# Kernel optimization log

Hardware: AMD Instinct MI355X
Metric: run time of the kernel (lower is better)

The kernel has to match this reference:

```python
import jax, jax.numpy as jnp
import numpy as np

L, H, NH, KVH, HD, DFF = 8, 1024, 16, 2, 64, 4096
G = NH // KVH          # kv groups = 8
S, PAST = 256, 2048
T = S + PAST
QKH = NH + KVH         # heads that receive RoPE


def setup_inputs() -> dict:
    key = jax.random.key(0)
    ks = jax.random.split(key, 10)
    w = 0.02
    # causal additive mask: past fully visible, causal within new chunk
    pos = jnp.arange(T)[None, :]
    mask = jnp.where(pos <= PAST + jnp.arange(S)[:, None], 0.0, -1e9).astype(jnp.float32)
    return {
        "hidden_states": jax.random.normal(ks[0], (S, H), jnp.float32),
        "rope_cos": jax.random.uniform(ks[1], (S, 1, HD), jnp.float32, -1.0, 1.0),
        "rope_sin": jax.random.uniform(ks[2], (S, 1, HD), jnp.float32, -1.0, 1.0),
        "attention_mask": mask,
        "past_keys": jax.random.normal(ks[3], (L, KVH, HD, PAST), jnp.float32),
        "past_values": jax.random.normal(ks[4], (L, KVH, PAST, HD), jnp.float32),
        "qkv_w": jax.random.normal(ks[5], (L, (NH + 2 * KVH) * HD, H), jnp.float32) * w,
        "o_w": jax.random.normal(ks[6], (L, H, H), jnp.float32) * w,
        "gate_up_w": jax.random.normal(ks[7], (L, 2 * DFF, H), jnp.float32) * w,
        "down_w": jax.random.normal(ks[8], (L, H, DFF), jnp.float32) * w,
        "norm_w": jnp.ones((H,), jnp.float32),
    }


def _rms_sum(x):
    # faithful to module: rsqrt of SUM of squares (sqrt(H) absorbed into fused weights)
    return x * jax.lax.rsqrt(jnp.sum(x * x, axis=-1, keepdims=True))


def _rotate_half(x):
    # flip-based rotate: swaps halves, NO negation (sign folded into sin input)
    return jnp.concatenate([x[..., HD // 2:], x[..., : HD // 2]], axis=-1)


def reference(hidden_states, rope_cos, rope_sin, attention_mask,
              past_keys, past_values, qkv_w, o_w, gate_up_w, down_w, norm_w):
    def layer(h, p):
        qw, ow, guw, dw, pk, pv = p
        # --- attention ---
        x = _rms_sum(h)
        qkv = (x @ qw.T).reshape(S, NH + 2 * KVH, HD)
        qk, v = qkv[:, :QKH], qkv[:, QKH:]               # [S,QKH,HD], [S,KVH,HD]
        qk = qk * rope_cos + _rotate_half(qk) * rope_sin
        q, k = qk[:, :NH], qk[:, NH:]
        q = q.reshape(S, KVH, G, HD).transpose(1, 2, 0, 3)       # [KVH,G,S,HD]
        K = jnp.concatenate([pk, k.transpose(1, 2, 0)], axis=-1)  # [KVH,HD,T]
        V = jnp.concatenate([pv, v.transpose(1, 0, 2)], axis=-2)  # [KVH,T,HD]
        scores = jnp.einsum('kgsd,kdt->kgst', q, K) + attention_mask
        p_attn = jax.nn.softmax(scores, axis=-1)
        o = jnp.einsum('kgst,ktd->kgsd', p_attn, V)
        o = o.transpose(2, 0, 1, 3).reshape(S, H)
        h = h + o @ ow.T
        # --- fused gate-up MLP (SiLU) ---
        x = _rms_sum(h)
        gu = x @ guw.T
        gate, up = gu[:, :DFF], gu[:, DFF:]
        h = h + (jax.nn.silu(gate) * up) @ dw.T
        return h, (K, V)

    h, _kv = jax.lax.scan(layer, hidden_states,
                          (qkv_w, o_w, gate_up_w, down_w, past_keys, past_values))
    # final RMSNorm (standard, mean-based, with learned weight)
    out = h * jax.lax.rsqrt(jnp.mean(h * h, axis=-1, keepdims=True) + 1e-6) * norm_w
    return out
```

## Files before the change

kernel.cpp:

```cpp
#include <hip/hip_runtime.h>
#include <hip/hip_bf16.h>

typedef __attribute__((ext_vector_type(4))) float f32x4;
typedef __attribute__((ext_vector_type(8))) __bf16 bf16x8;
typedef unsigned short u16;
typedef __attribute__((ext_vector_type(4))) unsigned short u16x4;
typedef __attribute__((ext_vector_type(8))) unsigned short u16x8;

__device__ __forceinline__ u16 f2bf(float f) {
  __bf16 h = (__bf16)f;
  return __builtin_bit_cast(u16, h);
}

__device__ __forceinline__ bf16x8 cvt2(f32x4 x, f32x4 y) {
  bf16x8 r;
  r[0] = (__bf16)x[0]; r[1] = (__bf16)x[1]; r[2] = (__bf16)x[2]; r[3] = (__bf16)x[3];
  r[4] = (__bf16)y[0]; r[5] = (__bf16)y[1]; r[6] = (__bf16)y[2]; r[7] = (__bf16)y[3];
  return r;
}

template<int CMODE, int NBK>
__global__ __launch_bounds__(512) void gemmW(
    const u16* __restrict__ A, const float* __restrict__ B,
    void* __restrict__ Cv, int K, int ldc)
{
  __shared__ char Bl[2][8192];
  int n0 = blockIdx.x * 32;
  int kb = blockIdx.y * (NBK * 128);
  int tid = threadIdx.x, lane = tid & 63, w = tid >> 6;
  int r0 = lane & 15, g = lane >> 4;
  int trow = tid >> 4, tcol = tid & 15;

  const float* bsrc = B + (long long)(n0 + trow) * K + kb + tcol * 8;
  const u16* abase = A + (long long)(w * 32 + r0) * K + kb + g * 8;
  int swr = (trow & 7) << 4;
  int wofs = trow * 256 + ((tcol * 16) ^ swr);

  {
    f32x4 u = *(const f32x4*)bsrc;
    f32x4 v = *(const f32x4*)(bsrc + 4);
    *(bf16x8*)&Bl[0][wofs] = cvt2(u, v);
  }
  bf16x8 a[2][2][4];
#pragma unroll
  for (int mi = 0; mi < 2; mi++)
#pragma unroll
    for (int kk = 0; kk < 4; kk++)
      a[0][mi][kk] = *(const bf16x8*)(abase + (long long)mi * 16 * K + kk * 32);

  f32x4 acc[2][2];
#pragma unroll
  for (int i = 0; i < 2; i++)
#pragma unroll
    for (int j = 0; j < 2; j++) acc[i][j] = (f32x4){0.f, 0.f, 0.f, 0.f};

  __syncthreads();

#pragma unroll
  for (int ibk = 0; ibk < NBK; ibk++) {
    const int cur = ibk & 1;
    const int nxt = cur ^ 1;
    f32x4 u, v;
    if (ibk + 1 < NBK) {
      int ko = (ibk + 1) * 128;
#pragma unroll
      for (int mi = 0; mi < 2; mi++)
#pragma unroll
        for (int kk = 0; kk < 4; kk++)
          a[nxt][mi][kk] = *(const bf16x8*)(abase + (long long)mi * 16 * K + ko + kk * 32);
      u = *(const f32x4*)(bsrc + ko);
      v = *(const f32x4*)(bsrc + ko + 4);
    }
    bf16x8 bfr[2][4];
#pragma unroll
    for (int nj = 0; nj < 2; nj++) {
      int row = nj * 16 + r0;
      int rb = row * 256, sw = (row & 7) << 4;
#pragma unroll
      for (int kk = 0; kk < 4; kk++)
        bfr[nj][kk] = *(const bf16x8*)&Bl[cur][rb + ((kk * 64 + g * 16) ^ sw)];
    }
#pragma unroll
    for (int kk = 0; kk < 4; kk++)
#pragma unroll
      for (int mi = 0; mi < 2; mi++)
#pragma unroll
        for (int nj = 0; nj < 2; nj++)
          acc[mi][nj] = __builtin_amdgcn_mfma_f32_16x16x32_bf16(a[cur][mi][kk], bfr[nj][kk], acc[mi][nj], 0, 0, 0);
    if (ibk + 1 < NBK)
      *(bf16x8*)&Bl[nxt][wofs] = cvt2(u, v);
    __syncthreads();
  }

  long long co = (long long)blockIdx.y * 256 * ldc;
  int rr = (lane >> 4) << 2;
#pragma unroll
  for (int mi = 0; mi < 2; mi++)
#pragma unroll
    for (int nj = 0; nj < 2; nj++)
#pragma unroll
      for (int q = 0; q < 4; q++) {
        int row = w * 32 + mi * 16 + rr + q;
        long long idx = co + (long long)row * ldc + n0 + nj * 16 + r0;
        float vv = acc[mi][nj][q];
        if (CMODE == 0) ((float*)Cv)[idx] = vv;
        else            ((u16*)Cv)[idx] = f2bf(vv);
      }
}

__global__ __launch_bounds__(256) void rms_fuse(const float* __restrict__ src,
                                                const float* __restrict__ parts, int np,
                                                float* __restrict__ hout, u16* __restrict__ x) {
  int s = blockIdx.x, tid = threadIdx.x;
  __shared__ float red[4];
  f32x4 hv = ((const f32x4*)(src + s * 1024))[tid];
  for (int p = 0; p < np; p++) {
    f32x4 pv = ((const f32x4*)(parts + (long long)p * 262144 + s * 1024))[tid];
    hv[0] += pv[0]; hv[1] += pv[1]; hv[2] += pv[2]; hv[3] += pv[3];
  }
  float ss = hv[0]*hv[0] + hv[1]*hv[1] + hv[2]*hv[2] + hv[3]*hv[3];
#pragma unroll
  for (int off = 32; off > 0; off >>= 1) ss += __shfl_xor(ss, off, 64);
  int lane = tid & 63, w = tid >> 6;
  if (lane == 0) red[w] = ss;
  __syncthreads();
  ss = red[0] + red[1] + red[2] + red[3];
  float r = 1.0f / sqrtf(ss);
  ((f32x4*)(hout + s * 1024))[tid] = hv;
  u16x4 o;
#pragma unroll
  for (int c = 0; c < 4; c++) o[c] = f2bf(hv[c] * r);
  ((u16x4*)x)[s * 256 + tid] = o;
}

__global__ __launch_bounds__(256) void final_fuse(const float* __restrict__ src,
                                                  const float* __restrict__ parts, int np,
                                                  const float* __restrict__ nw,
                                                  float* __restrict__ out) {
  int s = blockIdx.x, tid = threadIdx.x;
  __shared__ float red[4];
  f32x4 hv = ((const f32x4*)(src + s * 1024))[tid];
  for (int p = 0; p < np; p++) {
    f32x4 pv = ((const f32x4*)(parts + (long long)p * 262144 + s * 1024))[tid];
    hv[0] += pv[0]; hv[1] += pv[1]; hv[2] += pv[2]; hv[3] += pv[3];
  }
  float ss = hv[0]*hv[0] + hv[1]*hv[1] + hv[2]*hv[2] + hv[3]*hv[3];
#pragma unroll
  for (int off = 32; off > 0; off >>= 1) ss += __shfl_xor(ss, off, 64);
  int lane = tid & 63, w = tid >> 6;
  if (lane == 0) red[w] = ss;
  __syncthreads();
  ss = red[0] + red[1] + red[2] + red[3];
  float r = 1.0f / sqrtf(ss * (1.0f / 1024.0f) + 1e-6f);
  f32x4 wv = ((const f32x4*)nw)[tid];
  f32x4 o; o[0]=hv[0]*r*wv[0]; o[1]=hv[1]*r*wv[1]; o[2]=hv[2]*r*wv[2]; o[3]=hv[3]*r*wv[3];
  ((f32x4*)(out + s * 1024))[tid] = o;
}

__global__ __launch_bounds__(256) void transpose_past(const float* __restrict__ pk,
                                                      const float* __restrict__ pv,
                                                      u16* __restrict__ Kb, u16* __restrict__ Vb) {
  __shared__ float tile[64][65];
  int t0 = blockIdx.x * 64;
  int kvh = blockIdx.y;
  int l = blockIdx.z >> 1, part = blockIdx.z & 1;
  int lk = l * 2 + kvh;
  int tid = threadIdx.x;
  if (part == 0) {
    const float* src = pk + (long long)lk * 64 * 2048;
#pragma unroll
    for (int r = 0; r < 16; r++) {
      int idx = r * 256 + tid; int d = idx >> 6, t = idx & 63;
      tile[d][t] = src[d * 2048 + t0 + t];
    }
    __syncthreads();
    u16* dst = Kb + (long long)lk * 2304 * 64;
#pragma unroll
    for (int r = 0; r < 16; r++) {
      int idx = r * 256 + tid; int t = idx >> 6, d = idx & 63;
      dst[(t0 + t) * 64 + d] = f2bf(tile[d][t]);
    }
  } else {
    const float* src = pv + (long long)lk * 2048 * 64;
#pragma unroll
    for (int r = 0; r < 16; r++) {
      int idx = r * 256 + tid; int t = idx >> 6, d = idx & 63;
      tile[t][d] = src[(t0 + t) * 64 + d];
    }
    __syncthreads();
    u16* dst = Vb + (long long)lk * 64 * 2304;
#pragma unroll
    for (int r = 0; r < 16; r++) {
      int idx = r * 256 + tid; int d = idx >> 6, t = idx & 63;
      dst[d * 2304 + t0 + t] = f2bf(tile[t][d]);
    }
  }
}

__global__ __launch_bounds__(256) void rope_qkv(const float* __restrict__ P,
                                                const float* __restrict__ cs,
                                                const float* __restrict__ sn,
                                                u16* __restrict__ qb,
                                                u16* __restrict__ Kb,
                                                u16* __restrict__ Vb) {
  int s = blockIdx.x, tid = threadIdx.x;
  const float* p0 = P + (long long)s * 1280;
  const float* p1 = P + 327680 + (long long)s * 1280;
  for (int i = tid; i < 1280; i += 256) {
    int hh = i >> 6, d = i & 63;
    float v = p0[i] + p1[i];
    if (hh < 18) {
      int j = (hh << 6) | ((d + 32) & 63);
      float vr = p0[j] + p1[j];
      v = v * cs[s * 64 + d] + vr * sn[s * 64 + d];
      if (hh < 16) qb[hh * (256 * 64) + s * 64 + d] = f2bf(v);
      else         Kb[(hh - 16) * (2304 * 64) + (2048 + s) * 64 + d] = f2bf(v);
    } else {
      Vb[(hh - 18) * (64 * 2304) + d * 2304 + 2048 + s] = f2bf(v);
    }
  }
}

struct KV { bf16x8 kf[2][2]; bf16x8 vf[4]; };

__global__ __launch_bounds__(256) void flash_attn(
    const u16* __restrict__ qb, const u16* __restrict__ Kb2,
    const u16* __restrict__ Vb2, u16* __restrict__ oacc)
{
  __shared__ u16 Plds[4][16][36];
  __shared__ float Osh[4][16][68];
  __shared__ float msh[4][16];
  __shared__ float lsh[4][16];

  int hh = blockIdx.y, kvh = hh >> 3;
  int s0 = blockIdx.x * 16;
  int tid = threadIdx.x, lane = tid & 63, w = tid >> 6;
  int g = lane >> 4, r0 = lane & 15;

  const u16* Q  = qb  + hh * (256 * 64);
  const u16* Kh = Kb2 + kvh * (2304 * 64);
  const u16* Vh = Vb2 + kvh * (64 * 2304);

  bf16x8 qf[2];
#pragma unroll
  for (int kk = 0; kk < 2; kk++)
    qf[kk] = *(const bf16x8*)(Q + (s0 + r0) * 64 + kk * 32 + g * 8);

  f32x4 O[4];
#pragma unroll
  for (int dj = 0; dj < 4; dj++) O[dj] = (f32x4){0.f, 0.f, 0.f, 0.f};
  float m = -1e30f, l = 0.f;

  int t0s = w * 576;

  auto loadkv = [&](KV& d, int t0) {
#pragma unroll
    for (int tj = 0; tj < 2; tj++)
#pragma unroll
      for (int kk = 0; kk < 2; kk++)
        d.kf[tj][kk] = *(const bf16x8*)(Kh + (t0 + tj * 16 + r0) * 64 + kk * 32 + g * 8);
#pragma unroll
    for (int dj = 0; dj < 4; dj++)
      d.vf[dj] = *(const bf16x8*)(Vh + (dj * 16 + r0) * 2304 + t0 + g * 8);
  };

  auto step = [&](KV& kv, int t0) {
    f32x4 sc[2];
#pragma unroll
    for (int tj = 0; tj < 2; tj++) {
      f32x4 z = (f32x4){0.f, 0.f, 0.f, 0.f};
      z = __builtin_amdgcn_mfma_f32_16x16x32_bf16(kv.kf[tj][0], qf[0], z, 0, 0, 0);
      z = __builtin_amdgcn_mfma_f32_16x16x32_bf16(kv.kf[tj][1], qf[1], z, 0, 0, 0);
      sc[tj] = z;
    }
    if (t0 + 31 > 2048 + s0) {
#pragma unroll
      for (int tj = 0; tj < 2; tj++)
#pragma unroll
        for (int q = 0; q < 4; q++) {
          int tg = t0 + tj * 16 + g * 4 + q;
          int sg = s0 + r0;
          if (tg > 2048 + sg) sc[tj][q] = -1e30f;
        }
    }
    float rm = -1e30f;
#pragma unroll
    for (int tj = 0; tj < 2; tj++)
#pragma unroll
      for (int q = 0; q < 4; q++) rm = fmaxf(rm, sc[tj][q]);
    rm = fmaxf(rm, __shfl_xor(rm, 16, 64));
    rm = fmaxf(rm, __shfl_xor(rm, 32, 64));
    float mn = fmaxf(m, rm);
    float sca = __expf(m - mn);
    float rs = 0.f;
#pragma unroll
    for (int tj = 0; tj < 2; tj++)
#pragma unroll
      for (int q = 0; q < 4; q++) {
        sc[tj][q] = __expf(sc[tj][q] - mn);
        rs += sc[tj][q];
      }
    rs += __shfl_xor(rs, 16, 64);
    rs += __shfl_xor(rs, 32, 64);
    l = l * sca + rs;
    m = mn;
#pragma unroll
    for (int dj = 0; dj < 4; dj++) {
      O[dj][0] *= sca; O[dj][1] *= sca; O[dj][2] *= sca; O[dj][3] *= sca;
    }
#pragma unroll
    for (int tj = 0; tj < 2; tj++) {
      u16x4 pw;
#pragma unroll
      for (int q = 0; q < 4; q++) pw[q] = f2bf(sc[tj][q]);
      *(u16x4*)&Plds[w][r0][tj * 16 + g * 4] = pw;
    }
    u16x4 plo = *(const u16x4*)&Plds[w][r0][g * 8];
    u16x4 phi = *(const u16x4*)&Plds[w][r0][g * 8 + 4];
    union { bf16x8 v; u16x4 h[2]; } pu;
    pu.h[0] = plo; pu.h[1] = phi;
#pragma unroll
    for (int dj = 0; dj < 4; dj++)
      O[dj] = __builtin_amdgcn_mfma_f32_16x16x32_bf16(kv.vf[dj], pu.v, O[dj], 0, 0, 0);
  };

  KV bufA, bufB;
  loadkv(bufA, t0s);
#pragma unroll 1
  for (int it = 0; it < 18; it += 2) {
    int t0 = t0s + it * 32;
    loadkv(bufB, t0 + 32);
    step(bufA, t0);
    if (it + 2 < 18) loadkv(bufA, t0 + 64);
    step(bufB, t0 + 32);
  }

#pragma unroll
  for (int dj = 0; dj < 4; dj++)
    *(f32x4*)&Osh[w][r0][dj * 16 + g * 4] = O[dj];
  if (g == 0) { msh[w][r0] = m; lsh[w][r0] = l; }
  __syncthreads();

  int row = tid >> 4, c0 = (tid & 15) * 4;
  float M = fmaxf(fmaxf(msh[0][row], msh[1][row]), fmaxf(msh[2][row], msh[3][row]));
  float L = 0.f;
  float a0 = 0.f, a1 = 0.f, a2 = 0.f, a3 = 0.f;
#pragma unroll
  for (int w4 = 0; w4 < 4; w4++) {
    float e = __expf(msh[w4][row] - M);
    L += lsh[w4][row] * e;
    f32x4 ov = *(const f32x4*)&Osh[w4][row][c0];
    a0 += e * ov[0]; a1 += e * ov[1]; a2 += e * ov[2]; a3 += e * ov[3];
  }
  float inv = 1.0f / L;
  u16x4 o4;
  o4[0] = f2bf(a0 * inv); o4[1] = f2bf(a1 * inv);
  o4[2] = f2bf(a2 * inv); o4[3] = f2bf(a3 * inv);
  *(u16x4*)(oacc + (long long)(s0 + row) * 1024 + hh * 64 + c0) = o4;
}

__global__ __launch_bounds__(256) void silu_mul(const u16* __restrict__ gu, u16* __restrict__ y) {
  int t = blockIdx.x * 256 + threadIdx.x;
  int s = t >> 9, i8 = (t & 511) * 8;
  bf16x8 gv = *(const bf16x8*)(gu + s * 8192 + i8);
  bf16x8 uv = *(const bf16x8*)(gu + s * 8192 + 4096 + i8);
  u16x8 o8;
#pragma unroll
  for (int c = 0; c < 8; c++) {
    float gg = (float)gv[c];
    float uu = (float)uv[c];
    o8[c] = f2bf((gg / (1.0f + __expf(-gg))) * uu);
  }
  *(u16x8*)(y + s * 4096 + i8) = o8;
}

extern "C" void kernel_launch(void* const* d_in, const int* in_sizes, int n_in,
                              void* d_out, int out_size, void* d_ws, size_t ws_size,
                              hipStream_t stream) {
  (void)in_sizes; (void)n_in; (void)out_size; (void)ws_size;
  const float* hs   = (const float*)d_in[0];
  const float* rc   = (const float*)d_in[1];
  const float* rs   = (const float*)d_in[2];
  const float* pk   = (const float*)d_in[4];
  const float* pv   = (const float*)d_in[5];
  const float* qkvw = (const float*)d_in[6];
  const float* ow   = (const float*)d_in[7];
  const float* guw  = (const float*)d_in[8];
  const float* dw   = (const float*)d_in[9];
  const float* nw   = (const float*)d_in[10];
  float* out = (float*)d_out;

  char* base = (char*)d_ws;
  float* h   = (float*)(base + 0);
  u16*  x    = (u16*)(base + 1048576);
  float* Pq  = (float*)(base + 1572864);
  float* Po  = (float*)(base + 4194304);
  float* Pd  = (float*)(base + 8388608);
  u16*  gu   = (u16*)(base + 16777216);
  u16*  y    = (u16*)(base + 20971520);
  u16*  oacc = (u16*)(base + 23068672);
  u16*  qb   = (u16*)(base + 23592960);
  u16*  Kb   = (u16*)(base + 24117248);
  u16*  Vb   = (u16*)(base + 28835840);

  transpose_past<<<dim3(32, 2, 16), 256, 0, stream>>>(pk, pv, Kb, Vb);

  for (int l = 0; l < 8; ++l) {
    u16* Kbl = Kb + (long long)l * 2 * 2304 * 64;
    u16* Vbl = Vb + (long long)l * 2 * 64 * 2304;

    if (l == 0)
      rms_fuse<<<256, 256, 0, stream>>>(hs, nullptr, 0, h, x);
    else
      rms_fuse<<<256, 256, 0, stream>>>(h, Pd, 8, h, x);

    gemmW<0, 4><<<dim3(40, 2), 512, 0, stream>>>(
        x, qkvw + (long long)l * 1310720, Pq, 1024, 1280);
    rope_qkv<<<256, 256, 0, stream>>>(Pq, rc, rs, qb, Kbl, Vbl);
    flash_attn<<<dim3(16, 16), 256, 0, stream>>>(qb, Kbl, Vbl, oacc);
    gemmW<0, 2><<<dim3(32, 4), 512, 0, stream>>>(
        oacc, ow + (long long)l * 1048576, Po, 1024, 1024);
    rms_fuse<<<256, 256, 0, stream>>>(h, Po, 4, h, x);
    gemmW<1, 8><<<dim3(256, 1), 512, 0, stream>>>(
        x, guw + (long long)l * 8388608, gu, 1024, 8192);
    silu_mul<<<512, 256, 0, stream>>>(gu, y);
    gemmW<0, 4><<<dim3(32, 8), 512, 0, stream>>>(
        y, dw + (long long)l * 4194304, Pd, 4096, 1024);
  }
  final_fuse<<<256, 256, 0, stream>>>(h, Pd, 8, nw, out);
}
```

Before: 700.8 us.

## Fuse whole decoder stack into one cooperative persistent megakernel with grid barriers

Replaces the roughly 80 separate kernel launches (transpose, rms, gemms, rope, attention, silu) with one cooperative 256-block kernel. Phases are separated by atomic grid-wide barriers. The split-K and tiling layouts are reshaped to give 256 work units per phase, the SiLU multiply is fused into the gate-up GEMM epilogue, and attention uses 8 waves per block. This removes per-launch overhead and the intermediate gate-up buffer, at the cost of barrier spin latency and some idle blocks in phases with fewer tiles (QKV GEMM uses 160).

```diff
diff --git a/kernel.cpp b/kernel.cpp
--- a/kernel.cpp
+++ b/kernel.cpp
@@ -5,7 +5,6 @@
 typedef __attribute__((ext_vector_type(8))) __bf16 bf16x8;
 typedef unsigned short u16;
 typedef __attribute__((ext_vector_type(4))) unsigned short u16x4;
-typedef __attribute__((ext_vector_type(8))) unsigned short u16x8;
 
 __device__ __forceinline__ u16 f2bf(float f) {
   __bf16 h = (__bf16)f;
@@ -19,27 +18,50 @@
   return r;
 }
 
-template<int CMODE, int NBK>
-__global__ __launch_bounds__(512) void gemmW(
-    const u16* __restrict__ A, const float* __restrict__ B,
-    void* __restrict__ Cv, int K, int ldc)
-{
-  __shared__ char Bl[2][8192];
-  int n0 = blockIdx.x * 32;
-  int kb = blockIdx.y * (NBK * 128);
-  int tid = threadIdx.x, lane = tid & 63, w = tid >> 6;
+union Smem {
+  char gemmBl[2][8192];
+  struct {
+    u16 Plds[8][16][36];
+    float Osh[8][16][68];
+    float msh[8][16];
+    float lsh[8][16];
+  } fl;
+  float ttile[64][65];
+  float red[8];
+};
+
+struct MegaArgs {
+  const float *hs, *rc, *rs, *pk, *pv, *qkvw, *ow, *guw, *dw, *nw;
+  float* out;
+  char* ws;
+  int* bar;
+};
+
+__device__ __forceinline__ void gsync(int* bar, int ph) {
+  __syncthreads();
+  if (threadIdx.x == 0) {
+    __threadfence();
+    __hip_atomic_fetch_add(&bar[ph], 1, __ATOMIC_RELEASE, __HIP_MEMORY_SCOPE_AGENT);
+    while (__hip_atomic_load(&bar[ph], __ATOMIC_ACQUIRE, __HIP_MEMORY_SCOPE_AGENT) < (int)gridDim.x)
+      __builtin_amdgcn_s_sleep(8);
+    __threadfence();
+  }
+  __syncthreads();
+}
+
+template<int NBK>
+__device__ __forceinline__ void gemm_core(const u16* abase, const float* bsrc,
+                                          int K, Smem& sm, f32x4 acc[2][2]) {
+  int tid = threadIdx.x, lane = tid & 63;
   int r0 = lane & 15, g = lane >> 4;
   int trow = tid >> 4, tcol = tid & 15;
-
-  const float* bsrc = B + (long long)(n0 + trow) * K + kb + tcol * 8;
-  const u16* abase = A + (long long)(w * 32 + r0) * K + kb + g * 8;
   int swr = (trow & 7) << 4;
   int wofs = trow * 256 + ((tcol * 16) ^ swr);
 
   {
     f32x4 u = *(const f32x4*)bsrc;
     f32x4 v = *(const f32x4*)(bsrc + 4);
-    *(bf16x8*)&Bl[0][wofs] = cvt2(u, v);
+    *(bf16x8*)&sm.gemmBl[0][wofs] = cvt2(u, v);
   }
   bf16x8 a[2][2][4];
 #pragma unroll
@@ -48,7 +70,6 @@
     for (int kk = 0; kk < 4; kk++)
       a[0][mi][kk] = *(const bf16x8*)(abase + (long long)mi * 16 * K + kk * 32);
 
-  f32x4 acc[2][2];
 #pragma unroll
   for (int i = 0; i < 2; i++)
 #pragma unroll
@@ -78,7 +99,7 @@
       int rb = row * 256, sw = (row & 7) << 4;
 #pragma unroll
       for (int kk = 0; kk < 4; kk++)
-        bfr[nj][kk] = *(const bf16x8*)&Bl[cur][rb + ((kk * 64 + g * 16) ^ sw)];
+        bfr[nj][kk] = *(const bf16x8*)&sm.gemmBl[cur][rb + ((kk * 64 + g * 16) ^ sw)];
     }
 #pragma unroll
     for (int kk = 0; kk < 4; kk++)
@@ -88,158 +109,115 @@
         for (int nj = 0; nj < 2; nj++)
           acc[mi][nj] = __builtin_amdgcn_mfma_f32_16x16x32_bf16(a[cur][mi][kk], bfr[nj][kk], acc[mi][nj], 0, 0, 0);
     if (ibk + 1 < NBK)
-      *(bf16x8*)&Bl[nxt][wofs] = cvt2(u, v);
+      *(bf16x8*)&sm.gemmBl[nxt][wofs] = cvt2(u, v);
     __syncthreads();
   }
-
-  long long co = (long long)blockIdx.y * 256 * ldc;
-  int rr = (lane >> 4) << 2;
-#pragma unroll
-  for (int mi = 0; mi < 2; mi++)
-#pragma unroll
-    for (int nj = 0; nj < 2; nj++)
-#pragma unroll
-      for (int q = 0; q < 4; q++) {
-        int row = w * 32 + mi * 16 + rr + q;
-        long long idx = co + (long long)row * ldc + n0 + nj * 16 + r0;
-        float vv = acc[mi][nj][q];
-        if (CMODE == 0) ((float*)Cv)[idx] = vv;
-        else            ((u16*)Cv)[idx] = f2bf(vv);
-      }
-}
-
-__global__ __launch_bounds__(256) void rms_fuse(const float* __restrict__ src,
-                                                const float* __restrict__ parts, int np,
-                                                float* __restrict__ hout, u16* __restrict__ x) {
-  int s = blockIdx.x, tid = threadIdx.x;
-  __shared__ float red[4];
-  f32x4 hv = ((const f32x4*)(src + s * 1024))[tid];
-  for (int p = 0; p < np; p++) {
-    f32x4 pv = ((const f32x4*)(parts + (long long)p * 262144 + s * 1024))[tid];
-    hv[0] += pv[0]; hv[1] += pv[1]; hv[2] += pv[2]; hv[3] += pv[3];
+}
+
+__device__ void phase_rms(const float* src, const float* parts, int np,
+                          float* hout, u16* xout, Smem& sm) {
+  int s = blockIdx.x, tid = threadIdx.x, lane = tid & 63, w = tid >> 6;
+  f32x4 hv = (f32x4){0.f, 0.f, 0.f, 0.f};
+  if (tid < 256) {
+    hv = ((const f32x4*)(src + s * 1024))[tid];
+    for (int p = 0; p < np; p++) {
+      f32x4 pv = ((const f32x4*)(parts + (long long)p * 262144 + s * 1024))[tid];
+      hv[0] += pv[0]; hv[1] += pv[1]; hv[2] += pv[2]; hv[3] += pv[3];
+    }
   }
   float ss = hv[0]*hv[0] + hv[1]*hv[1] + hv[2]*hv[2] + hv[3]*hv[3];
 #pragma unroll
   for (int off = 32; off > 0; off >>= 1) ss += __shfl_xor(ss, off, 64);
-  int lane = tid & 63, w = tid >> 6;
-  if (lane == 0) red[w] = ss;
-  __syncthreads();
-  ss = red[0] + red[1] + red[2] + red[3];
+  if (lane == 0) sm.red[w] = ss;
+  __syncthreads();
+  ss = sm.red[0] + sm.red[1] + sm.red[2] + sm.red[3];
   float r = 1.0f / sqrtf(ss);
-  ((f32x4*)(hout + s * 1024))[tid] = hv;
-  u16x4 o;
-#pragma unroll
-  for (int c = 0; c < 4; c++) o[c] = f2bf(hv[c] * r);
-  ((u16x4*)x)[s * 256 + tid] = o;
-}
-
-__global__ __launch_bounds__(256) void final_fuse(const float* __restrict__ src,
-                                                  const float* __restrict__ parts, int np,
-                                                  const float* __restrict__ nw,
-                                                  float* __restrict__ out) {
-  int s = blockIdx.x, tid = threadIdx.x;
-  __shared__ float red[4];
-  f32x4 hv = ((const f32x4*)(src + s * 1024))[tid];
-  for (int p = 0; p < np; p++) {
-    f32x4 pv = ((const f32x4*)(parts + (long long)p * 262144 + s * 1024))[tid];
-    hv[0] += pv[0]; hv[1] += pv[1]; hv[2] += pv[2]; hv[3] += pv[3];
+  if (tid < 256) {
+    ((f32x4*)(hout + s * 1024))[tid] = hv;
+    u16x4 o;
+#pragma unroll
+    for (int c = 0; c < 4; c++) o[c] = f2bf(hv[c] * r);
+    ((u16x4*)xout)[s * 256 + tid] = o;
+  }
+}
+
+__device__ void phase_final(const float* src, const float* parts,
+                            const float* nw, float* out, Smem& sm) {
+  int s = blockIdx.x, tid = threadIdx.x, lane = tid & 63, w = tid >> 6;
+  f32x4 hv = (f32x4){0.f, 0.f, 0.f, 0.f};
+  if (tid < 256) {
+    hv = ((const f32x4*)(src + s * 1024))[tid];
+    for (int p = 0; p < 8; p++) {
+      f32x4 pv = ((const f32x4*)(parts + (long long)p * 262144 + s * 1024))[tid];
+      hv[0] += pv[0]; hv[1] += pv[1]; hv[2] += pv[2]; hv[3] += pv[3];
+    }
   }
   float ss = hv[0]*hv[0] + hv[1]*hv[1] + hv[2]*hv[2] + hv[3]*hv[3];
 #pragma unroll
   for (int off = 32; off > 0; off >>= 1) ss += __shfl_xor(ss, off, 64);
-  int lane = tid & 63, w = tid >> 6;
-  if (lane == 0) red[w] = ss;
-  __syncthreads();
-  ss = red[0] + red[1] + red[2] + red[3];
+  if (lane == 0) sm.red[w] = ss;
+  __syncthreads();
+  ss = sm.red[0] + sm.red[1] + sm.red[2] + sm.red[3];
   float r = 1.0f / sqrtf(ss * (1.0f / 1024.0f) + 1e-6f);
-  f32x4 wv = ((const f32x4*)nw)[tid];
-  f32x4 o; o[0]=hv[0]*r*wv[0]; o[1]=hv[1]*r*wv[1]; o[2]=hv[2]*r*wv[2]; o[3]=hv[3]*r*wv[3];
-  ((f32x4*)(out + s * 1024))[tid] = o;
-}
-
-__global__ __launch_bounds__(256) void transpose_past(const float* __restrict__ pk,
-                                                      const float* __restrict__ pv,
-                                                      u16* __restrict__ Kb, u16* __restrict__ Vb) {
-  __shared__ float tile[64][65];
-  int t0 = blockIdx.x * 64;
-  int kvh = blockIdx.y;
-  int l = blockIdx.z >> 1, part = blockIdx.z & 1;
+  if (tid < 256) {
+    f32x4 wv = ((const f32x4*)nw)[tid];
+    f32x4 o;
+    o[0]=hv[0]*r*wv[0]; o[1]=hv[1]*r*wv[1]; o[2]=hv[2]*r*wv[2]; o[3]=hv[3]*r*wv[3];
+    ((f32x4*)(out + s * 1024))[tid] = o;
+  }
+}
+
+__device__ void transpose_unit(int unit, const float* pk, const float* pv,
+                               u16* Kb, u16* Vb, Smem& sm) {
+  int xt = unit & 31, rest = unit >> 5;
+  int kvh = rest & 1, z = rest >> 1;
+  int l = z >> 1, part = z & 1;
   int lk = l * 2 + kvh;
-  int tid = threadIdx.x;
+  int t0 = xt * 64, tid = threadIdx.x;
   if (part == 0) {
-    const float* src = pk + (long long)lk * 64 * 2048;
-#pragma unroll
-    for (int r = 0; r < 16; r++) {
-      int idx = r * 256 + tid; int d = idx >> 6, t = idx & 63;
-      tile[d][t] = src[d * 2048 + t0 + t];
+    const float* src = pk + (long long)lk * 131072;
+#pragma unroll
+    for (int r = 0; r < 8; r++) {
+      int idx = r * 512 + tid; int d = idx >> 6, t = idx & 63;
+      sm.ttile[d][t] = src[d * 2048 + t0 + t];
     }
     __syncthreads();
-    u16* dst = Kb + (long long)lk * 2304 * 64;
-#pragma unroll
-    for (int r = 0; r < 16; r++) {
-      int idx = r * 256 + tid; int t = idx >> 6, d = idx & 63;
-      dst[(t0 + t) * 64 + d] = f2bf(tile[d][t]);
+    u16* dst = Kb + (long long)lk * 147456;
+#pragma unroll
+    for (int r = 0; r < 8; r++) {
+      int idx = r * 512 + tid; int t = idx >> 6, d = idx & 63;
+      dst[(t0 + t) * 64 + d] = f2bf(sm.ttile[d][t]);
     }
   } else {
-    const float* src = pv + (long long)lk * 2048 * 64;
-#pragma unroll
-    for (int r = 0; r < 16; r++) {
-      int idx = r * 256 + tid; int t = idx >> 6, d = idx & 63;
-      tile[t][d] = src[(t0 + t) * 64 + d];
+    const float* src = pv + (long long)lk * 131072;
+#pragma unroll
+    for (int r = 0; r < 8; r++) {
+      int idx = r * 512 + tid; int t = idx >> 6, d = idx & 63;
+      sm.ttile[t][d] = src[(t0 + t) * 64 + d];
     }
     __syncthreads();
-    u16* dst = Vb + (long long)lk * 64 * 2304;
-#pragma unroll
-    for (int r = 0; r < 16; r++) {
-      int idx = r * 256 + tid; int d = idx >> 6, t = idx & 63;
-      dst[d * 2304 + t0 + t] = f2bf(tile[t][d]);
-    }
-  }
-}
-
-__global__ __launch_bounds__(256) void rope_qkv(const float* __restrict__ P,
-                                                const float* __restrict__ cs,
-                                                const float* __restrict__ sn,
-                                                u16* __restrict__ qb,
-                                                u16* __restrict__ Kb,
-                                                u16* __restrict__ Vb) {
-  int s = blockIdx.x, tid = threadIdx.x;
-  const float* p0 = P + (long long)s * 1280;
-  const float* p1 = P + 327680 + (long long)s * 1280;
-  for (int i = tid; i < 1280; i += 256) {
-    int hh = i >> 6, d = i & 63;
-    float v = p0[i] + p1[i];
-    if (hh < 18) {
-      int j = (hh << 6) | ((d + 32) & 63);
-      float vr = p0[j] + p1[j];
-      v = v * cs[s * 64 + d] + vr * sn[s * 64 + d];
-      if (hh < 16) qb[hh * (256 * 64) + s * 64 + d] = f2bf(v);
-      else         Kb[(hh - 16) * (2304 * 64) + (2048 + s) * 64 + d] = f2bf(v);
-    } else {
-      Vb[(hh - 18) * (64 * 2304) + d * 2304 + 2048 + s] = f2bf(v);
-    }
-  }
+    u16* dst = Vb + (long long)lk * 147456;
+#pragma unroll
+    for (int r = 0; r < 8; r++) {
+      int idx = r * 512 + tid; int d = idx >> 6, t = idx & 63;
+      dst[d * 2304 + t0 + t] = f2bf(sm.ttile[t][d]);
+    }
+  }
+  __syncthreads();
 }
 
 struct KV { bf16x8 kf[2][2]; bf16x8 vf[4]; };
 
-__global__ __launch_bounds__(256) void flash_attn(
-    const u16* __restrict__ qb, const u16* __restrict__ Kb2,
-    const u16* __restrict__ Vb2, u16* __restrict__ oacc)
-{
-  __shared__ u16 Plds[4][16][36];
-  __shared__ float Osh[4][16][68];
-  __shared__ float msh[4][16];
-  __shared__ float lsh[4][16];
-
-  int hh = blockIdx.y, kvh = hh >> 3;
-  int s0 = blockIdx.x * 16;
-  int tid = threadIdx.x, lane = tid & 63, w = tid >> 6;
+__device__ void phase_flash(const u16* qb, const u16* Kb2, const u16* Vb2,
+                            u16* oacc, Smem& sm) {
+  int bid = blockIdx.x, tid = threadIdx.x, lane = tid & 63, w = tid >> 6;
   int g = lane >> 4, r0 = lane & 15;
-
-  const u16* Q  = qb  + hh * (256 * 64);
-  const u16* Kh = Kb2 + kvh * (2304 * 64);
-  const u16* Vh = Vb2 + kvh * (64 * 2304);
+  int hh = bid & 15, qt = bid >> 4;
+  int s0 = qt * 16, kvh = hh >> 3;
+
+  const u16* Q  = qb  + hh * 16384;
+  const u16* Kh = Kb2 + kvh * 147456;
+  const u16* Vh = Vb2 + kvh * 147456;
 
   bf16x8 qf[2];
 #pragma unroll
@@ -251,7 +229,7 @@
   for (int dj = 0; dj < 4; dj++) O[dj] = (f32x4){0.f, 0.f, 0.f, 0.f};
   float m = -1e30f, l = 0.f;
 
-  int t0s = w * 576;
+  int t0s = w * 288;
 
   auto loadkv = [&](KV& d, int t0) {
 #pragma unroll
@@ -313,10 +291,10 @@
       u16x4 pw;
 #pragma unroll
       for (int q = 0; q < 4; q++) pw[q] = f2bf(sc[tj][q]);
-      *(u16x4*)&Plds[w][r0][tj * 16 + g * 4] = pw;
-    }
-    u16x4 plo = *(const u16x4*)&Plds[w][r0][g * 8];
-    u16x4 phi = *(const u16x4*)&Plds[w][r0][g * 8 + 4];
+      *(u16x4*)&sm.fl.Plds[w][r0][tj * 16 + g * 4] = pw;
+    }
+    u16x4 plo = *(const u16x4*)&sm.fl.Plds[w][r0][g * 8];
+    u16x4 phi = *(const u16x4*)&sm.fl.Plds[w][r0][g * 8 + 4];
     union { bf16x8 v; u16x4 h[2]; } pu;
     pu.h[0] = plo; pu.h[1] = phi;
 #pragma unroll
@@ -324,108 +302,212 @@
       O[dj] = __builtin_amdgcn_mfma_f32_16x16x32_bf16(kv.vf[dj], pu.v, O[dj], 0, 0, 0);
   };
 
-  KV bufA, bufB;
-  loadkv(bufA, t0s);
+  KV ba, bb;
+  loadkv(ba, t0s);
 #pragma unroll 1
-  for (int it = 0; it < 18; it += 2) {
-    int t0 = t0s + it * 32;
-    loadkv(bufB, t0 + 32);
-    step(bufA, t0);
-    if (it + 2 < 18) loadkv(bufA, t0 + 64);
-    step(bufB, t0 + 32);
-  }
+  for (int p = 0; p < 4; p++) {
+    int t0 = t0s + p * 64;
+    loadkv(bb, t0 + 32);
+    step(ba, t0);
+    loadkv(ba, t0 + 64);
+    step(bb, t0 + 32);
+  }
+  step(ba, t0s + 256);
 
 #pragma unroll
   for (int dj = 0; dj < 4; dj++)
-    *(f32x4*)&Osh[w][r0][dj * 16 + g * 4] = O[dj];
-  if (g == 0) { msh[w][r0] = m; lsh[w][r0] = l; }
-  __syncthreads();
-
-  int row = tid >> 4, c0 = (tid & 15) * 4;
-  float M = fmaxf(fmaxf(msh[0][row], msh[1][row]), fmaxf(msh[2][row], msh[3][row]));
-  float L = 0.f;
-  float a0 = 0.f, a1 = 0.f, a2 = 0.f, a3 = 0.f;
-#pragma unroll
-  for (int w4 = 0; w4 < 4; w4++) {
-    float e = __expf(msh[w4][row] - M);
-    L += lsh[w4][row] * e;
-    f32x4 ov = *(const f32x4*)&Osh[w4][row][c0];
-    a0 += e * ov[0]; a1 += e * ov[1]; a2 += e * ov[2]; a3 += e * ov[3];
-  }
-  float inv = 1.0f / L;
-  u16x4 o4;
-  o4[0] = f2bf(a0 * inv); o4[1] = f2bf(a1 * inv);
-  o4[2] = f2bf(a2 * inv); o4[3] = f2bf(a3 * inv);
-  *(u16x4*)(oacc + (long long)(s0 + row) * 1024 + hh * 64 + c0) = o4;
-}
-
-__global__ __launch_bounds__(256) void silu_mul(const u16* __restrict__ gu, u16* __restrict__ y) {
-  int t = blockIdx.x * 256 + threadIdx.x;
-  int s = t >> 9, i8 = (t & 511) * 8;
-  bf16x8 gv = *(const bf16x8*)(gu + s * 8192 + i8);
-  bf16x8 uv = *(const bf16x8*)(gu + s * 8192 + 4096 + i8);
-  u16x8 o8;
-#pragma unroll
-  for (int c = 0; c < 8; c++) {
-    float gg = (float)gv[c];
-    float uu = (float)uv[c];
-    o8[c] = f2bf((gg / (1.0f + __expf(-gg))) * uu);
-  }
-  *(u16x8*)(y + s * 4096 + i8) = o8;
+    *(f32x4*)&sm.fl.Osh[w][r0][dj * 16 + g * 4] = O[dj];
+  if (g == 0) { sm.fl.msh[w][r0] = m; sm.fl.lsh[w][r0] = l; }
+  __syncthreads();
+
+  if (tid < 256) {
+    int row = tid >> 4, c0 = (tid & 15) * 4;
+    float M = -1e30f;
+#pragma unroll
+    for (int w8 = 0; w8 < 8; w8++) M = fmaxf(M, sm.fl.msh[w8][row]);
+    float L = 0.f;
+    float a0 = 0.f, a1 = 0.f, a2 = 0.f, a3 = 0.f;
+#pragma unroll
+    for (int w8 = 0; w8 < 8; w8++) {
+      float e = __expf(sm.fl.msh[w8][row] - M);
+      L += sm.fl.lsh[w8][row] * e;
+      f32x4 ov = *(const f32x4*)&sm.fl.Osh[w8][row][c0];
+      a0 += e * ov[0]; a1 += e * ov[1]; a2 += e * ov[2]; a3 += e * ov[3];
+    }
+    float inv = 1.0f / L;
+    u16x4 o4;
+    o4[0] = f2bf(a0 * inv); o4[1] = f2bf(a1 * inv);
+    o4[2] = f2bf(a2 * inv); o4[3] = f2bf(a3 * inv);
+    *(u16x4*)(oacc + (long long)(s0 + row) * 1024 + hh * 64 + c0) = o4;
+  }
+}
+
+__global__ __launch_bounds__(512, 2) void mega(MegaArgs A) {
+  __shared__ Smem sm;
+  int* bar = A.bar;
+  int ph = 0;
+  const int bid = blockIdx.x, tid = threadIdx.x;
+  const int lane = tid & 63, w = tid >> 6;
+  const int r0 = lane & 15, g = lane >> 4;
+  const int trow = tid >> 4, tcol = tid & 15;
+  const int rr = (lane >> 4) << 2;
+
+  char* ws = A.ws;
+  float* h    = (float*)(ws);
+  u16*   x    = (u16*)(ws + 1048576);
+  float* Pq   = (float*)(ws + 1572864);
+  float* Po   = (float*)(ws + 6815744);
+  float* Pd   = (float*)(ws + 15204352);
+  u16*   y    = (u16*)(ws + 23592960);
+  u16*   oacc = (u16*)(ws + 25690112);
+  u16*   qb   = (u16*)(ws + 26214400);
+  u16*   Kb   = (u16*)(ws + 26738688);
+  u16*   Vb   = (u16*)(ws + 31457280);
+
+  for (int u = 0; u < 4; u++)
+    transpose_unit(bid * 4 + u, A.pk, A.pv, Kb, Vb, sm);
+  gsync(bar, ph++);
+
+  for (int l = 0; l < 8; l++) {
+    const float* qkvw_l = A.qkvw + (long long)l * 1310720;
+    const float* ow_l   = A.ow   + (long long)l * 1048576;
+    const float* guw_l  = A.guw  + (long long)l * 8388608;
+    const float* dw_l   = A.dw   + (long long)l * 4194304;
+    u16* Kbl = Kb + (long long)l * 294912;
+    u16* Vbl = Vb + (long long)l * 294912;
+
+    phase_rms(l == 0 ? A.hs : h, Pd, l == 0 ? 0 : 8, h, x, sm);
+    gsync(bar, ph++);
+
+    if (bid < 160) {
+      int nt = bid % 40, slab = bid / 40;
+      int n0 = nt * 32, kb = slab * 256;
+      const u16* abase = x + (long long)(w * 32 + r0) * 1024 + g * 8 + kb;
+      const float* bsrc = qkvw_l + (long long)(n0 + trow) * 1024 + kb + tcol * 8;
+      f32x4 acc[2][2];
+      gemm_core<2>(abase, bsrc, 1024, sm, acc);
+      float* dst = Pq + (long long)slab * 327680;
+#pragma unroll
+      for (int mi = 0; mi < 2; mi++)
+#pragma unroll
+        for (int nj = 0; nj < 2; nj++)
+#pragma unroll
+          for (int q = 0; q < 4; q++) {
+            int row = w * 32 + mi * 16 + rr + q;
+            dst[row * 1280 + n0 + nj * 16 + r0] = acc[mi][nj][q];
+          }
+    }
+    gsync(bar, ph++);
+
+    {
+      int s = bid;
+      for (int i = tid; i < 1280; i += 512) {
+        int hh = i >> 6, d = i & 63;
+        long long o0 = (long long)s * 1280;
+        float v = Pq[o0 + i] + Pq[327680 + o0 + i] + Pq[655360 + o0 + i] + Pq[983040 + o0 + i];
+        if (hh < 18) {
+          int j = (hh << 6) | ((d + 32) & 63);
+          float vr = Pq[o0 + j] + Pq[327680 + o0 + j] + Pq[655360 + o0 + j] + Pq[983040 + o0 + j];
+          v = v * A.rc[s * 64 + d] + vr * A.rs[s * 64 + d];
+          if (hh < 16) qb[hh * 16384 + s * 64 + d] = f2bf(v);
+          else         Kbl[(hh - 16) * 147456 + (2048 + s) * 64 + d] = f2bf(v);
+        } else {
+          Vbl[(hh - 18) * 147456 + d * 2304 + 2048 + s] = f2bf(v);
+        }
+      }
+    }
+    gsync(bar, ph++);
+
+    phase_flash(qb, Kbl, Vbl, oacc, sm);
+    gsync(bar, ph++);
+
+    {
+      int n_idx = bid & 31, slab = bid >> 5;
+      int n0 = n_idx * 32, kb = slab * 128;
+      const u16* abase = oacc + (long long)(w * 32 + r0) * 1024 + g * 8 + kb;
+      const float* bsrc = ow_l + (long long)(n0 + trow) * 1024 + kb + tcol * 8;
+      f32x4 acc[2][2];
+      gemm_core<1>(abase, bsrc, 1024, sm, acc);
+      float* dst = Po + (long long)slab * 262144;
+#pragma unroll
+      for (int mi = 0; mi < 2; mi++)
+#pragma unroll
+        for (int nj = 0; nj < 2; nj++)
+#pragma unroll
+          for (int q = 0; q < 4; q++) {
+            int row = w * 32 + mi * 16 + rr + q;
+            dst[row * 1024 + n0 + nj * 16 + r0] = acc[mi][nj][q];
+          }
+    }
+    gsync(bar, ph++);
+
+    phase_rms(h, Po, 8, h, x, sm);
+    gsync(bar, ph++);
+
+    {
+      int n0 = bid * 16;
+      const u16* abase = x + (long long)(w * 32 + r0) * 1024 + g * 8;
+      const float* brow = (trow < 16)
+          ? (guw_l + (long long)(n0 + trow) * 1024)
+          : (guw_l + (long long)(4096 + n0 + trow - 16) * 1024);
+      const float* bsrc = brow + tcol * 8;
+      f32x4 acc[2][2];
+      gemm_core<8>(abase, bsrc, 1024, sm, acc);
+#pragma unroll
+      for (int mi = 0; mi < 2; mi++)
+#pragma unroll
+        for (int q = 0; q < 4; q++) {
+          int row = w * 32 + mi * 16 + rr + q;
+          float gv = acc[mi][0][q], uv = acc[mi][1][q];
+          y[(long long)row * 4096 + n0 + r0] = f2bf((gv / (1.0f + __expf(-gv))) * uv);
+        }
+    }
+    gsync(bar, ph++);
+
+    {
+      int n_idx = bid & 31, slab = bid >> 5;
+      int n0 = n_idx * 32, kb = slab * 512;
+      const u16* abase = y + (long long)(w * 32 + r0) * 4096 + g * 8 + kb;
+      const float* bsrc = dw_l + (long long)(n0 + trow) * 4096 + kb + tcol * 8;
+      f32x4 acc[2][2];
+      gemm_core<4>(abase, bsrc, 4096, sm, acc);
+      float* dst = Pd + (long long)slab * 262144;
+#pragma unroll
+      for (int mi = 0; mi < 2; mi++)
+#pragma unroll
+        for (int nj = 0; nj < 2; nj++)
+#pragma unroll
+          for (int q = 0; q < 4; q++) {
+            int row = w * 32 + mi * 16 + rr + q;
+            dst[row * 1024 + n0 + nj * 16 + r0] = acc[mi][nj][q];
+          }
+    }
+    gsync(bar, ph++);
+  }
+
+  phase_final(h, Pd, A.nw, A.out, sm);
 }
 
 extern "C" void kernel_launch(void* const* d_in, const int* in_sizes, int n_in,
                               void* d_out, int out_size, void* d_ws, size_t ws_size,
                               hipStream_t stream) {
   (void)in_sizes; (void)n_in; (void)out_size; (void)ws_size;
-  const float* hs   = (const float*)d_in[0];
-  const float* rc   = (const float*)d_in[1];
-  const float* rs   = (const float*)d_in[2];
-  const float* pk   = (const float*)d_in[4];
-  const float* pv   = (const float*)d_in[5];
-  const float* qkvw = (const float*)d_in[6];
-  const float* ow   = (const float*)d_in[7];
-  const float* guw  = (const float*)d_in[8];
-  const float* dw   = (const float*)d_in[9];
-  const float* nw   = (const float*)d_in[10];
-  float* out = (float*)d_out;
-
-  char* base = (char*)d_ws;
-  float* h   = (float*)(base + 0);
-  u16*  x    = (u16*)(base + 1048576);
-  float* Pq  = (float*)(base + 1572864);
-  float* Po  = (float*)(base + 4194304);
-  float* Pd  = (float*)(base + 8388608);
-  u16*  gu   = (u16*)(base + 16777216);
-  u16*  y    = (u16*)(base + 20971520);
-  u16*  oacc = (u16*)(base + 23068672);
-  u16*  qb   = (u16*)(base + 23592960);
-  u16*  Kb   = (u16*)(base + 24117248);
-  u16*  Vb   = (u16*)(base + 28835840);
-
-  transpose_past<<<dim3(32, 2, 16), 256, 0, stream>>>(pk, pv, Kb, Vb);
-
-  for (int l = 0; l < 8; ++l) {
-    u16* Kbl = Kb + (long long)l * 2 * 2304 * 64;
-    u16* Vbl = Vb + (long long)l * 2 * 64 * 2304;
-
-    if (l == 0)
-      rms_fuse<<<256, 256, 0, stream>>>(hs, nullptr, 0, h, x);
-    else
-      rms_fuse<<<256, 256, 0, stream>>>(h, Pd, 8, h, x);
-
-    gemmW<0, 4><<<dim3(40, 2), 512, 0, stream>>>(
-        x, qkvw + (long long)l * 1310720, Pq, 1024, 1280);
-    rope_qkv<<<256, 256, 0, stream>>>(Pq, rc, rs, qb, Kbl, Vbl);
-    flash_attn<<<dim3(16, 16), 256, 0, stream>>>(qb, Kbl, Vbl, oacc);
-    gemmW<0, 2><<<dim3(32, 4), 512, 0, stream>>>(
-        oacc, ow + (long long)l * 1048576, Po, 1024, 1024);
-    rms_fuse<<<256, 256, 0, stream>>>(h, Po, 4, h, x);
-    gemmW<1, 8><<<dim3(256, 1), 512, 0, stream>>>(
-        x, guw + (long long)l * 8388608, gu, 1024, 8192);
-    silu_mul<<<512, 256, 0, stream>>>(gu, y);
-    gemmW<0, 4><<<dim3(32, 8), 512, 0, stream>>>(
-        y, dw + (long long)l * 4194304, Pd, 4096, 1024);
-  }
-  final_fuse<<<256, 256, 0, stream>>>(h, Pd, 8, nw, out);
-}
+  MegaArgs ma;
+  ma.hs   = (const float*)d_in[0];
+  ma.rc   = (const float*)d_in[1];
+  ma.rs   = (const float*)d_in[2];
+  ma.pk   = (const float*)d_in[4];
+  ma.pv   = (const float*)d_in[5];
+  ma.qkvw = (const float*)d_in[6];
+  ma.ow   = (const float*)d_in[7];
+  ma.guw  = (const float*)d_in[8];
+  ma.dw   = (const float*)d_in[9];
+  ma.nw   = (const float*)d_in[10];
+  ma.out  = (float*)d_out;
+  ma.ws   = (char*)d_ws;
+  ma.bar  = (int*)((char*)d_ws + 36175872);
+
+  hipMemsetAsync((char*)d_ws + 36175872, 0, 1024, stream);
+  void* kargs[] = { (void*)&ma };
+  hipLaunchCooperativeKernel((const void*)mega, dim3(256), dim3(512), kargs, 0, stream);
+}
```

Result: slower. 2.718 ms (+287.9%).
